# Kernel optimization log

Measured on AMD Instinct MI355X. Metric: run time of the kernel, lower is better.

Reference implementation:

```python
import jax, jax.numpy as jnp
import numpy as np

B, H, W, C = 4, 128, 128, 256
D_MODEL, NH = 512, 8
DH = D_MODEL // NH  # 64


def setup_inputs() -> dict:
    key = jax.random.key(0)
    ks = jax.random.split(key, 5)
    s = lambda fan_in: 1.0 / np.sqrt(fan_in)
    return {
        "x": jax.random.normal(ks[0], (B, H, W, C), jnp.float32),
        "Wq": jax.random.normal(ks[1], (C, D_MODEL), jnp.float32) * s(C),
        "bq": jnp.zeros((D_MODEL,), jnp.float32),
        "Wk": jax.random.normal(ks[2], (C, D_MODEL), jnp.float32) * s(C),
        "bk": jnp.zeros((D_MODEL,), jnp.float32),
        "Wv": jax.random.normal(ks[3], (C, D_MODEL), jnp.float32) * s(C),
        "bv": jnp.zeros((D_MODEL,), jnp.float32),
        "Wo": jax.random.normal(ks[4], (D_MODEL, C), jnp.float32) * s(D_MODEL),
        "bo": jnp.zeros((C,), jnp.float32),
    }


def reference(x, Wq, bq, Wk, bk, Wv, bv, Wo, bo):
    # Axial multi-head attention along axis 1 (H), W axis is batched.
    b, h, w, _ = x.shape
    q = (x @ Wq + bq).reshape(b, h, w, NH, DH) * (DH ** -0.5)
    k = (x @ Wk + bk).reshape(b, h, w, NH, DH)
    v = (x @ Wv + bv).reshape(b, h, w, NH, DH)
    # scores over the H axis: [B, Nh, W, H, H]
    scores = jnp.einsum("bxwnd,bywnd->bnwxy", q, k)
    probs = jax.nn.softmax(scores, axis=-1)
    # [B, H, W, Nh, DH] -> [B, H, W, d_model]
    out = jnp.einsum("bnwxy,bywnd->bxwnd", probs, v).reshape(b, h, w, D_MODEL)
    # Wo projection; original combines to [B,W,H,C] then permutes back to [B,H,W,C],
    # which is equivalent to applying Wo directly here. Dropout is identity at inference.
    return out @ Wo + bo
```

## Files before the change

kernel.cpp:

```cpp
#include <hip/hip_runtime.h>

typedef unsigned short u16;
typedef __attribute__((ext_vector_type(8))) short bf16x8;
typedef __attribute__((ext_vector_type(8))) unsigned short u16x8;
typedef __attribute__((ext_vector_type(4))) float f32x4;

#define DEVI static __device__ __forceinline__

DEVI u16 f2b(float f) {
  unsigned u = __builtin_bit_cast(unsigned, f);
  return (u16)((u + 0x7FFFu + ((u >> 16) & 1u)) >> 16);
}

DEVI void gload_lds16(const void* g, void* l) {
  __builtin_amdgcn_global_load_lds(
      (const __attribute__((address_space(1))) unsigned int*)g,
      (__attribute__((address_space(3))) unsigned int*)l, 16, 0, 0);
}


__global__ __launch_bounds__(256) void prep_x(const float* __restrict__ x, u16* __restrict__ xb) {
  const int n8 = 65536 * 256 / 8;
  int i = blockIdx.x * blockDim.x + threadIdx.x;
  for (; i < n8; i += gridDim.x * blockDim.x) {
    const float4* p = (const float4*)x + (size_t)i * 2;
    float4 a = p[0], b = p[1];
    u16x8 r;
    r[0] = f2b(a.x); r[1] = f2b(a.y); r[2] = f2b(a.z); r[3] = f2b(a.w);
    r[4] = f2b(b.x); r[5] = f2b(b.y); r[6] = f2b(b.z); r[7] = f2b(b.w);
    *(u16x8*)(xb + (size_t)i * 8) = r;
  }
}

__global__ __launch_bounds__(256) void prep_w(
    const float* __restrict__ Wq, const float* __restrict__ Wk,
    const float* __restrict__ Wv, const float* __restrict__ Wo,
    const float* __restrict__ bq, const float* __restrict__ bk, const float* __restrict__ bv,
    u16* __restrict__ wqkvT, u16* __restrict__ woT, float* __restrict__ bqkv) {
  const int NW1 = 1536 * 256, NW2 = 256 * 512;
  const int total = NW1 + NW2 + 1536;
  int i = blockIdx.x * blockDim.x + threadIdx.x;
  for (; i < total; i += gridDim.x * blockDim.x) {
    if (i < NW1) {
      int nn = i >> 8, kk = i & 255;
      float v;
      if (nn < 512)       v = Wq[kk * 512 + nn] * 0.125f;
      else if (nn < 1024) v = Wk[kk * 512 + (nn - 512)];
      else                v = Wv[kk * 512 + (nn - 1024)];
      wqkvT[i] = f2b(v);
    } else if (i < NW1 + NW2) {
      int j = i - NW1;
      int nn = j >> 9, kk = j & 511;
      woT[j] = f2b(Wo[kk * 256 + nn]);
    } else {
      int j = i - NW1 - NW2;
      bqkv[j] = (j < 512) ? bq[j] * 0.125f : (j < 1024 ? bk[j - 512] : bv[j - 1024]);
    }
  }
}


template <int KK, bool OUT_BF16>
__global__ __launch_bounds__(512, 2) void gemm256(
    const u16* __restrict__ A, const u16* __restrict__ Bt,
    const float* __restrict__ bias, void* __restrict__ Cv, int N) {
  constexpr int NT = KK / 64;
  __shared__ u16 smem[65536];
  const int tid = threadIdx.x;
  const int lane = tid & 63, wid = tid >> 6;
  const int nTn = N >> 8;
  const int qx = gridDim.x >> 3;
  const int wg = (blockIdx.x & 7) * qx + (blockIdx.x >> 3);
  const long m0 = (long)(wg / nTn) * 256;
  const long n0 = (long)(wg % nTn) * 256;
  const int wr = wid >> 2, wc = wid & 3;
  const int hi = lane >> 4, lo = lane & 15;
  const u16* Ab = A + m0 * KK;
  const u16* Bb = Bt + n0 * KK;
  const int srow_ = tid >> 3;
  const int schunk = tid & 7;

  f32x4 acc[8][4];
#pragma unroll
  for (int mi = 0; mi < 8; ++mi)
#pragma unroll
    for (int ni = 0; ni < 4; ++ni) acc[mi][ni] = f32x4{0.f, 0.f, 0.f, 0.f};

  auto stage = [&](int t) {
    u16* base = &smem[(t & 1) * 32768];
    const int kt = t * 64;
#pragma unroll
    for (int j = 0; j < 4; ++j) {
      int row = j * 64 + srow_;
      int colE = (schunk ^ (row & 7)) << 3;
      gload_lds16(Ab + (long)row * KK + kt + colE, &base[(j * 512 + tid) * 8]);
    }
#pragma unroll
    for (int j = 0; j < 4; ++j) {
      int row = j * 64 + srow_;
      int colE = (schunk ^ (row & 7)) << 3;
      gload_lds16(Bb + (long)row * KK + kt + colE, &base[16384 + (j * 512 + tid) * 8]);
    }
  };

  stage(0);
#pragma unroll
  for (int t = 0; t < NT; ++t) {
    if (t + 1 < NT) {
      stage(t + 1);
      asm volatile("s_waitcnt vmcnt(8)" ::: "memory");
    } else {
      asm volatile("s_waitcnt vmcnt(0)" ::: "memory");
    }
    __builtin_amdgcn_sched_barrier(0);
    __builtin_amdgcn_s_barrier();
    const u16* aB = &smem[(t & 1) * 32768];
    const u16* bB = aB + 16384;
#pragma unroll
    for (int ks = 0; ks < 2; ++ks) {
      const int slot = ((hi + ks * 4) ^ (lo & 7)) << 3;
      bf16x8 af[8], bfr[4];
#pragma unroll
      for (int mi = 0; mi < 8; ++mi)
        af[mi] = *(const bf16x8*)&aB[(wr * 128 + mi * 16 + lo) * 64 + slot];
#pragma unroll
      for (int ni = 0; ni < 4; ++ni)
        bfr[ni] = *(const bf16x8*)&bB[(wc * 64 + ni * 16 + lo) * 64 + slot];
#pragma unroll
      for (int mi = 0; mi < 8; ++mi)
#pragma unroll
        for (int ni = 0; ni < 4; ++ni)
          acc[mi][ni] = __builtin_amdgcn_mfma_f32_16x16x32_bf16(af[mi], bfr[ni], acc[mi][ni], 0, 0, 0);
    }
    __builtin_amdgcn_sched_barrier(0);
    __builtin_amdgcn_s_barrier();
  }

  float bb[4];
#pragma unroll
  for (int ni = 0; ni < 4; ++ni) bb[ni] = bias[n0 + wc * 64 + ni * 16 + lo];

  if (OUT_BF16) {
    u16* Cg = (u16*)Cv;
#pragma unroll
    for (int h = 0; h < 2; ++h) {
      if (wr == h) {
#pragma unroll
        for (int mi = 0; mi < 8; ++mi)
#pragma unroll
          for (int ni = 0; ni < 4; ++ni) {
            int cl = wc * 64 + ni * 16 + lo;
#pragma unroll
            for (int j = 0; j < 4; ++j)
              smem[(mi * 16 + hi * 4 + j) * 256 + cl] = f2b(acc[mi][ni][j] + bb[ni]);
          }
      }
      __syncthreads();
#pragma unroll
      for (int it = 0; it < 8; ++it) {
        int idx = it * 512 + tid;
        int row = idx >> 5, col8 = (idx & 31) * 8;
        *(u16x8*)(Cg + (m0 + h * 128 + row) * N + n0 + col8) = *(const u16x8*)&smem[row * 256 + col8];
      }
      __syncthreads();
    }
  } else {
    float* Cg = (float*)Cv;
#pragma unroll
    for (int mi = 0; mi < 8; ++mi)
#pragma unroll
      for (int ni = 0; ni < 4; ++ni) {
        long cg = n0 + wc * 64 + ni * 16 + lo;
#pragma unroll
        for (int j = 0; j < 4; ++j)
          Cg[(m0 + wr * 128 + mi * 16 + hi * 4 + j) * N + cg] = acc[mi][ni][j] + bb[ni];
      }
  }
}


__global__ __launch_bounds__(256) void attn_axial(const u16* __restrict__ qkv,
                                                  u16* __restrict__ ao) {
  __shared__ u16 smem[24576];
  u16* qld = smem;
  u16* kld = smem + 8192;
  u16* vt  = smem + 16384;
  u16* pld = smem;

  const int g = blockIdx.x;
  const int n = g & 7, w = (g >> 3) & 127, b = g >> 10;
  const int tid = threadIdx.x, lane = tid & 63, wid = tid >> 6;
  const size_t ystr = (size_t)128 * 1536;
  const size_t base = (size_t)(b * 16384 + w) * 1536;
  const size_t bq_ = base + n * 64;
  const size_t bk_ = base + 512 + n * 64;
  const size_t bv_ = base + 1024 + n * 64;
  const int srow = lane >> 3, sc = lane & 7;
  const int hi = lane >> 4, lo = lane & 15;

#pragma unroll
  for (int j = 0; j < 4; ++j) {
    int y = wid * 32 + j * 8 + srow;
    gload_lds16(qkv + bq_ + (size_t)y * ystr + sc * 8, &qld[(wid * 32 + j * 8) * 64]);
    gload_lds16(qkv + bk_ + (size_t)y * ystr + sc * 8, &kld[(wid * 32 + j * 8) * 64]);
  }
  {
    const int h2 = tid >> 6;
    const int yp = (tid & 63) * 2;
    const u16* g0 = qkv + bv_ + (size_t)yp * ystr + h2 * 16;
    u16x8 a0 = *(const u16x8*)g0;
    u16x8 a1 = *(const u16x8*)(g0 + 8);
    u16x8 c0 = *(const u16x8*)(g0 + ystr);
    u16x8 c1 = *(const u16x8*)(g0 + ystr + 8);
    unsigned* vt32 = (unsigned*)vt;
#pragma unroll
    for (int e = 0; e < 8; ++e) {
      vt32[(h2 * 16 + e) * 64 + (yp >> 1)]     = (unsigned)a0[e] | ((unsigned)c0[e] << 16);
      vt32[(h2 * 16 + 8 + e) * 64 + (yp >> 1)] = (unsigned)a1[e] | ((unsigned)c1[e] << 16);
    }
  }
  __syncthreads();

  f32x4 s[2][8];
#pragma unroll
  for (int mi = 0; mi < 2; ++mi)
#pragma unroll
    for (int ni = 0; ni < 8; ++ni) s[mi][ni] = f32x4{0.f, 0.f, 0.f, 0.f};
#pragma unroll
  for (int ks = 0; ks < 2; ++ks) {
    bf16x8 aq[2];
#pragma unroll
    for (int mi = 0; mi < 2; ++mi)
      aq[mi] = *(const bf16x8*)&qld[(wid * 32 + mi * 16 + lo) * 64 + hi * 8 + ks * 32];
#pragma unroll
    for (int ni = 0; ni < 8; ++ni) {
      bf16x8 bk2 = *(const bf16x8*)&kld[(ni * 16 + lo) * 64 + hi * 8 + ks * 32];
#pragma unroll
      for (int mi = 0; mi < 2; ++mi)
        s[mi][ni] = __builtin_amdgcn_mfma_f32_16x16x32_bf16(aq[mi], bk2, s[mi][ni], 0, 0, 0);
    }
  }
  __syncthreads();

  float rinv[2][4];
  u16* pw = &pld[wid * 32 * 128];
#pragma unroll
  for (int mi = 0; mi < 2; ++mi) {
#pragma unroll
    for (int j = 0; j < 4; ++j) {
      float m = s[mi][0][j];
#pragma unroll
      for (int ni = 1; ni < 8; ++ni) m = fmaxf(m, s[mi][ni][j]);
#pragma unroll
      for (int d = 1; d < 16; d <<= 1) m = fmaxf(m, __shfl_xor(m, d, 64));
      float sum = 0.f;
#pragma unroll
      for (int ni = 0; ni < 8; ++ni) {
        float e = exp2f((s[mi][ni][j] - m) * 1.44269504f);
        s[mi][ni][j] = e;
        sum += e;
      }
#pragma unroll
      for (int d = 1; d < 16; d <<= 1) sum += __shfl_xor(sum, d, 64);
      rinv[mi][j] = 1.f / sum;
      const int q = mi * 16 + hi * 4 + j;
#pragma unroll
      for (int ni = 0; ni < 8; ++ni)
        pw[q * 128 + ni * 16 + lo] = f2b(s[mi][ni][j]);
    }
  }

  f32x4 o[2][4];
#pragma unroll
  for (int mi = 0; mi < 2; ++mi)
#pragma unroll
    for (int ni = 0; ni < 4; ++ni) o[mi][ni] = f32x4{0.f, 0.f, 0.f, 0.f};
#pragma unroll
  for (int ks = 0; ks < 4; ++ks) {
    bf16x8 ap[2];
#pragma unroll
    for (int mi = 0; mi < 2; ++mi)
      ap[mi] = *(const bf16x8*)&pw[(mi * 16 + lo) * 128 + hi * 8 + ks * 32];
#pragma unroll
    for (int ni = 0; ni < 4; ++ni) {
      bf16x8 bv2 = *(const bf16x8*)&vt[(ni * 16 + lo) * 128 + hi * 8 + ks * 32];
#pragma unroll
      for (int mi = 0; mi < 2; ++mi)
        o[mi][ni] = __builtin_amdgcn_mfma_f32_16x16x32_bf16(ap[mi], bv2, o[mi][ni], 0, 0, 0);
    }
  }

#pragma unroll
  for (int mi = 0; mi < 2; ++mi)
#pragma unroll
    for (int j = 0; j < 4; ++j) {
      const int q = wid * 32 + mi * 16 + hi * 4 + j;
      const size_t obase = ((size_t)(b * 16384 + q * 128 + w)) * 512 + (size_t)n * 64;
#pragma unroll
      for (int ni = 0; ni < 4; ++ni)
        ao[obase + ni * 16 + lo] = f2b(o[mi][ni][j] * rinv[mi][j]);
    }
}


extern "C" void kernel_launch(void* const* d_in, const int* in_sizes, int n_in,
                              void* d_out, int out_size, void* d_ws, size_t ws_size,
                              hipStream_t stream) {
  (void)in_sizes; (void)n_in; (void)out_size; (void)ws_size;
  const float* x  = (const float*)d_in[0];
  const float* Wq = (const float*)d_in[1];
  const float* bq = (const float*)d_in[2];
  const float* Wk = (const float*)d_in[3];
  const float* bk = (const float*)d_in[4];
  const float* Wv = (const float*)d_in[5];
  const float* bv = (const float*)d_in[6];
  const float* Wo = (const float*)d_in[7];
  const float* bo = (const float*)d_in[8];
  float* out = (float*)d_out;

  char* ws = (char*)d_ws;
  const size_t MiB = (size_t)1 << 20;
  u16* qkv   = (u16*)ws;
  u16* xb    = (u16*)(ws + 192 * MiB);
  u16* wqkvT = (u16*)(ws + 224 * MiB);
  u16* woT   = wqkvT + 1536 * 256;
  float* bqkv = (float*)(woT + 256 * 512);

  prep_x<<<2048, 256, 0, stream>>>(x, xb);
  prep_w<<<512, 256, 0, stream>>>(Wq, Wk, Wv, Wo, bq, bk, bv, wqkvT, woT, bqkv);

  gemm256<256, true><<<1536, 512, 0, stream>>>(xb, wqkvT, bqkv, qkv, 1536);
  attn_axial<<<4096, 256, 0, stream>>>(qkv, (u16*)out);
  gemm256<512, false><<<256, 512, 0, stream>>>((const u16*)out, woT, bo, out, 256);
}
```

Measured before the change: 219.9 us.

## Fuse QKV projection, axial attention and output projection into one kernel

Replaces the five-kernel pipeline (x conversion, QKV GEMM, attention, Wo GEMM) with one fused kernel per (batch, column). Each block converts its x column to bf16 in LDS, computes Q, K and V per head from pre-swizzled weight pieces streamed through double-buffered LDS, runs softmax attention, and accumulates the Wo projection in registers. The K bias is dropped because it cancels in softmax, and the V bias is folded into a precomputed output bias. This removes the large qkv and intermediate HBM round-trips and the extra launches, at the cost of only 512 blocks, heavy LDS use and many barriers per head.

```diff
diff --git a/kernel.cpp b/kernel.cpp
--- a/kernel.cpp
+++ b/kernel.cpp
@@ -3,6 +3,7 @@
 typedef unsigned short u16;
 typedef __attribute__((ext_vector_type(8))) short bf16x8;
 typedef __attribute__((ext_vector_type(8))) unsigned short u16x8;
+typedef __attribute__((ext_vector_type(4))) unsigned short u16x4;
 typedef __attribute__((ext_vector_type(4))) float f32x4;
 
 #define DEVI static __device__ __forceinline__
@@ -18,287 +19,320 @@
       (__attribute__((address_space(3))) unsigned int*)l, 16, 0, 0);
 }
 
-
-__global__ __launch_bounds__(256) void prep_x(const float* __restrict__ x, u16* __restrict__ xb) {
-  const int n8 = 65536 * 256 / 8;
-  int i = blockIdx.x * blockDim.x + threadIdx.x;
-  for (; i < n8; i += gridDim.x * blockDim.x) {
-    const float4* p = (const float4*)x + (size_t)i * 2;
-    float4 a = p[0], b = p[1];
-    u16x8 r;
-    r[0] = f2b(a.x); r[1] = f2b(a.y); r[2] = f2b(a.z); r[3] = f2b(a.w);
-    r[4] = f2b(b.x); r[5] = f2b(b.y); r[6] = f2b(b.z); r[7] = f2b(b.w);
-    *(u16x8*)(xb + (size_t)i * 8) = r;
-  }
-}
-
-__global__ __launch_bounds__(256) void prep_w(
+#define LGKM0 asm volatile("s_waitcnt lgkmcnt(0)" ::: "memory")
+#define VMW(N) asm volatile("s_waitcnt vmcnt(" #N ")" ::: "memory")
+DEVI void sbar() {
+  __builtin_amdgcn_sched_barrier(0);
+  __builtin_amdgcn_s_barrier();
+  __builtin_amdgcn_sched_barrier(0);
+}
+DEVI bf16x8 mfma_ld(const u16* p) { return *(const bf16x8*)p; }
+
+__global__ __launch_bounds__(256) void prep_w2(
     const float* __restrict__ Wq, const float* __restrict__ Wk,
     const float* __restrict__ Wv, const float* __restrict__ Wo,
-    const float* __restrict__ bq, const float* __restrict__ bk, const float* __restrict__ bv,
-    u16* __restrict__ wqkvT, u16* __restrict__ woT, float* __restrict__ bqkv) {
-  const int NW1 = 1536 * 256, NW2 = 256 * 512;
-  const int total = NW1 + NW2 + 1536;
+    const float* __restrict__ bq, const float* __restrict__ bv,
+    const float* __restrict__ bo, u16* __restrict__ img,
+    float* __restrict__ bqv, float* __restrict__ bo2) {
+  const int NW = 524288;
+  const int total = NW + 512 + 256;
   int i = blockIdx.x * blockDim.x + threadIdx.x;
   for (; i < total; i += gridDim.x * blockDim.x) {
-    if (i < NW1) {
-      int nn = i >> 8, kk = i & 255;
+    if (i < NW) {
+      const int piece = i >> 14, r = i & 16383;
+      const int h = piece >> 2, wh = piece & 3;
       float v;
-      if (nn < 512)       v = Wq[kk * 512 + nn] * 0.125f;
-      else if (nn < 1024) v = Wk[kk * 512 + (nn - 512)];
-      else                v = Wv[kk * 512 + (nn - 1024)];
-      wqkvT[i] = f2b(v);
-    } else if (i < NW1 + NW2) {
-      int j = i - NW1;
-      int nn = j >> 9, kk = j & 511;
-      woT[j] = f2b(Wo[kk * 256 + nn]);
+      if (wh < 3) {
+        const int n = r >> 8, cpos = (r >> 3) & 31, e = r & 7;
+        const int k = ((cpos ^ (n & 7)) << 3) + e;
+        const int col = h * 64 + n;
+        v = (wh == 0) ? Wq[k * 512 + col] * 0.125f
+          : (wh == 1) ? Wk[k * 512 + col] : Wv[k * 512 + col];
+      } else {
+        const int cc = r >> 6, cpos = (r >> 3) & 7, e = r & 7;
+        const int kk = ((cpos ^ (cc & 7)) << 3) + e;
+        v = Wo[(h * 64 + kk) * 256 + cc];
+      }
+      img[i] = f2b(v);
+    } else if (i < NW + 512) {
+      const int j = i - NW;
+      bqv[j] = bq[j] * 0.125f;
     } else {
-      int j = i - NW1 - NW2;
-      bqkv[j] = (j < 512) ? bq[j] * 0.125f : (j < 1024 ? bk[j - 512] : bv[j - 1024]);
+      const int j = i - NW - 512;
+      float acc = bo[j];
+      for (int dd = 0; dd < 512; ++dd) acc += bv[dd] * Wo[dd * 256 + j];
+      bo2[j] = acc;
     }
   }
 }
 
 
-template <int KK, bool OUT_BF16>
-__global__ __launch_bounds__(512, 2) void gemm256(
-    const u16* __restrict__ A, const u16* __restrict__ Bt,
-    const float* __restrict__ bias, void* __restrict__ Cv, int N) {
-  constexpr int NT = KK / 64;
-  __shared__ u16 smem[65536];
-  const int tid = threadIdx.x;
-  const int lane = tid & 63, wid = tid >> 6;
-  const int nTn = N >> 8;
-  const int qx = gridDim.x >> 3;
-  const int wg = (blockIdx.x & 7) * qx + (blockIdx.x >> 3);
-  const long m0 = (long)(wg / nTn) * 256;
-  const long n0 = (long)(wg % nTn) * 256;
-  const int wr = wid >> 2, wc = wid & 3;
-  const int hi = lane >> 4, lo = lane & 15;
-  const u16* Ab = A + m0 * KK;
-  const u16* Bb = Bt + n0 * KK;
-  const int srow_ = tid >> 3;
-  const int schunk = tid & 7;
-
-  f32x4 acc[8][4];
-#pragma unroll
-  for (int mi = 0; mi < 8; ++mi)
-#pragma unroll
-    for (int ni = 0; ni < 4; ++ni) acc[mi][ni] = f32x4{0.f, 0.f, 0.f, 0.f};
-
-  auto stage = [&](int t) {
-    u16* base = &smem[(t & 1) * 32768];
-    const int kt = t * 64;
-#pragma unroll
-    for (int j = 0; j < 4; ++j) {
-      int row = j * 64 + srow_;
-      int colE = (schunk ^ (row & 7)) << 3;
-      gload_lds16(Ab + (long)row * KK + kt + colE, &base[(j * 512 + tid) * 8]);
-    }
-#pragma unroll
-    for (int j = 0; j < 4; ++j) {
-      int row = j * 64 + srow_;
-      int colE = (schunk ^ (row & 7)) << 3;
-      gload_lds16(Bb + (long)row * KK + kt + colE, &base[16384 + (j * 512 + tid) * 8]);
-    }
-  };
-
-  stage(0);
-#pragma unroll
-  for (int t = 0; t < NT; ++t) {
-    if (t + 1 < NT) {
-      stage(t + 1);
-      asm volatile("s_waitcnt vmcnt(8)" ::: "memory");
-    } else {
-      asm volatile("s_waitcnt vmcnt(0)" ::: "memory");
-    }
-    __builtin_amdgcn_sched_barrier(0);
-    __builtin_amdgcn_s_barrier();
-    const u16* aB = &smem[(t & 1) * 32768];
-    const u16* bB = aB + 16384;
-#pragma unroll
-    for (int ks = 0; ks < 2; ++ks) {
-      const int slot = ((hi + ks * 4) ^ (lo & 7)) << 3;
-      bf16x8 af[8], bfr[4];
-#pragma unroll
-      for (int mi = 0; mi < 8; ++mi)
-        af[mi] = *(const bf16x8*)&aB[(wr * 128 + mi * 16 + lo) * 64 + slot];
-#pragma unroll
-      for (int ni = 0; ni < 4; ++ni)
-        bfr[ni] = *(const bf16x8*)&bB[(wc * 64 + ni * 16 + lo) * 64 + slot];
-#pragma unroll
-      for (int mi = 0; mi < 8; ++mi)
-#pragma unroll
-        for (int ni = 0; ni < 4; ++ni)
-          acc[mi][ni] = __builtin_amdgcn_mfma_f32_16x16x32_bf16(af[mi], bfr[ni], acc[mi][ni], 0, 0, 0);
-    }
-    __builtin_amdgcn_sched_barrier(0);
-    __builtin_amdgcn_s_barrier();
-  }
-
-  float bb[4];
-#pragma unroll
-  for (int ni = 0; ni < 4; ++ni) bb[ni] = bias[n0 + wc * 64 + ni * 16 + lo];
-
-  if (OUT_BF16) {
-    u16* Cg = (u16*)Cv;
-#pragma unroll
-    for (int h = 0; h < 2; ++h) {
-      if (wr == h) {
-#pragma unroll
-        for (int mi = 0; mi < 8; ++mi)
-#pragma unroll
-          for (int ni = 0; ni < 4; ++ni) {
-            int cl = wc * 64 + ni * 16 + lo;
-#pragma unroll
-            for (int j = 0; j < 4; ++j)
-              smem[(mi * 16 + hi * 4 + j) * 256 + cl] = f2b(acc[mi][ni][j] + bb[ni]);
-          }
-      }
-      __syncthreads();
-#pragma unroll
-      for (int it = 0; it < 8; ++it) {
-        int idx = it * 512 + tid;
-        int row = idx >> 5, col8 = (idx & 31) * 8;
-        *(u16x8*)(Cg + (m0 + h * 128 + row) * N + n0 + col8) = *(const u16x8*)&smem[row * 256 + col8];
-      }
-      __syncthreads();
-    }
-  } else {
-    float* Cg = (float*)Cv;
-#pragma unroll
-    for (int mi = 0; mi < 8; ++mi)
-#pragma unroll
-      for (int ni = 0; ni < 4; ++ni) {
-        long cg = n0 + wc * 64 + ni * 16 + lo;
-#pragma unroll
-        for (int j = 0; j < 4; ++j)
-          Cg[(m0 + wr * 128 + mi * 16 + hi * 4 + j) * N + cg] = acc[mi][ni][j] + bb[ni];
-      }
-  }
-}
-
-
-__global__ __launch_bounds__(256) void attn_axial(const u16* __restrict__ qkv,
-                                                  u16* __restrict__ ao) {
-  __shared__ u16 smem[24576];
-  u16* qld = smem;
-  u16* kld = smem + 8192;
-  u16* vt  = smem + 16384;
-  u16* pld = smem;
+__global__ __launch_bounds__(512) void fused_axial(
+    const float* __restrict__ x, const u16* __restrict__ img,
+    const float* __restrict__ bqv, const float* __restrict__ bo2,
+    float* __restrict__ out) {
+  __shared__ u16 lds[73728];
+  const int WB0 = 0, WB1 = 16384, QB = 32768, KB = 40960, VT = 49152, PB = 57344;
+  const int XO = 32768;
 
   const int g = blockIdx.x;
-  const int n = g & 7, w = (g >> 3) & 127, b = g >> 10;
+  const int b = g >> 7, w = g & 127;
   const int tid = threadIdx.x, lane = tid & 63, wid = tid >> 6;
-  const size_t ystr = (size_t)128 * 1536;
-  const size_t base = (size_t)(b * 16384 + w) * 1536;
-  const size_t bq_ = base + n * 64;
-  const size_t bk_ = base + 512 + n * 64;
-  const size_t bv_ = base + 1024 + n * 64;
-  const int srow = lane >> 3, sc = lane & 7;
-  const int hi = lane >> 4, lo = lane & 15;
-
-#pragma unroll
-  for (int j = 0; j < 4; ++j) {
-    int y = wid * 32 + j * 8 + srow;
-    gload_lds16(qkv + bq_ + (size_t)y * ystr + sc * 8, &qld[(wid * 32 + j * 8) * 64]);
-    gload_lds16(qkv + bk_ + (size_t)y * ystr + sc * 8, &kld[(wid * 32 + j * 8) * 64]);
-  }
+  const int s = wid >> 1, nh = wid & 1;
+  const int lo = lane & 15, hi = lane >> 4;
+  const int l8 = lo & 7;
+
   {
-    const int h2 = tid >> 6;
-    const int yp = (tid & 63) * 2;
-    const u16* g0 = qkv + bv_ + (size_t)yp * ystr + h2 * 16;
-    u16x8 a0 = *(const u16x8*)g0;
-    u16x8 a1 = *(const u16x8*)(g0 + 8);
-    u16x8 c0 = *(const u16x8*)(g0 + ystr);
-    u16x8 c1 = *(const u16x8*)(g0 + ystr + 8);
-    unsigned* vt32 = (unsigned*)vt;
-#pragma unroll
-    for (int e = 0; e < 8; ++e) {
-      vt32[(h2 * 16 + e) * 64 + (yp >> 1)]     = (unsigned)a0[e] | ((unsigned)c0[e] << 16);
-      vt32[(h2 * 16 + 8 + e) * 64 + (yp >> 1)] = (unsigned)a1[e] | ((unsigned)c1[e] << 16);
+    const int y = tid >> 2, q4 = tid & 3;
+    const float4* xr = (const float4*)(x + ((size_t)((b * 128 + y) * 128 + w)) * 256) + q4 * 16;
+#pragma unroll
+    for (int c8 = 0; c8 < 8; ++c8) {
+      float4 f0 = xr[c8 * 2], f1 = xr[c8 * 2 + 1];
+      u16x8 r;
+      r[0] = f2b(f0.x); r[1] = f2b(f0.y); r[2] = f2b(f0.z); r[3] = f2b(f0.w);
+      r[4] = f2b(f1.x); r[5] = f2b(f1.y); r[6] = f2b(f1.z); r[7] = f2b(f1.w);
+      *(u16x8*)&lds[XO + y * 256 + (((q4 * 8 + c8) ^ (y & 7)) << 3)] = r;
     }
   }
   __syncthreads();
 
-  f32x4 s[2][8];
-#pragma unroll
-  for (int mi = 0; mi < 2; ++mi)
-#pragma unroll
-    for (int ni = 0; ni < 8; ++ni) s[mi][ni] = f32x4{0.f, 0.f, 0.f, 0.f};
-#pragma unroll
-  for (int ks = 0; ks < 2; ++ks) {
-    bf16x8 aq[2];
-#pragma unroll
-    for (int mi = 0; mi < 2; ++mi)
-      aq[mi] = *(const bf16x8*)&qld[(wid * 32 + mi * 16 + lo) * 64 + hi * 8 + ks * 32];
-#pragma unroll
-    for (int ni = 0; ni < 8; ++ni) {
-      bf16x8 bk2 = *(const bf16x8*)&kld[(ni * 16 + lo) * 64 + hi * 8 + ks * 32];
-#pragma unroll
-      for (int mi = 0; mi < 2; ++mi)
-        s[mi][ni] = __builtin_amdgcn_mfma_f32_16x16x32_bf16(aq[mi], bk2, s[mi][ni], 0, 0, 0);
-    }
+  bf16x8 areg[2][8];
+#pragma unroll
+  for (int m = 0; m < 2; ++m)
+#pragma unroll
+    for (int k8 = 0; k8 < 8; ++k8)
+      areg[m][k8] = mfma_ld(&lds[XO + (s * 32 + m * 16 + lo) * 256 + (((k8 * 4 + hi) ^ l8) << 3)]);
+
+  auto stagep = [&](int piece) {
+    const u16* src = img + (size_t)piece * 16384;
+    u16* dst = &lds[(piece & 1) ? WB1 : WB0];
+#pragma unroll
+    for (int it = 0; it < 4; ++it)
+      gload_lds16(src + (it * 512 + tid) * 8, dst + (it * 512 + tid) * 8);
+  };
+
+  stagep(0);
+  float bqa = bqv[nh * 32 + lo], bqb = bqv[nh * 32 + 16 + lo];
+
+  f32x4 oacc[2][8];
+#pragma unroll
+  for (int m = 0; m < 2; ++m)
+#pragma unroll
+    for (int n = 0; n < 8; ++n) oacc[m][n] = f32x4{0.f, 0.f, 0.f, 0.f};
+
+  LGKM0;
+  sbar();
+
+  for (int h = 0; h < 8; ++h) {
+    const int p0 = h * 4;
+
+    stagep(p0 + 1);
+    VMW(4); sbar();
+    {
+      f32x4 ga[2][2];
+#pragma unroll
+      for (int m = 0; m < 2; ++m)
+#pragma unroll
+        for (int n = 0; n < 2; ++n) ga[m][n] = f32x4{0.f, 0.f, 0.f, 0.f};
+#pragma unroll
+      for (int k8 = 0; k8 < 8; ++k8) {
+        bf16x8 bf0 = mfma_ld(&lds[WB0 + (nh * 32 + lo) * 256 + (((k8 * 4 + hi) ^ l8) << 3)]);
+        bf16x8 bf1 = mfma_ld(&lds[WB0 + (nh * 32 + 16 + lo) * 256 + (((k8 * 4 + hi) ^ l8) << 3)]);
+#pragma unroll
+        for (int m = 0; m < 2; ++m) {
+          ga[m][0] = __builtin_amdgcn_mfma_f32_16x16x32_bf16(areg[m][k8], bf0, ga[m][0], 0, 0, 0);
+          ga[m][1] = __builtin_amdgcn_mfma_f32_16x16x32_bf16(areg[m][k8], bf1, ga[m][1], 0, 0, 0);
+        }
+      }
+#pragma unroll
+      for (int n = 0; n < 2; ++n) {
+        const int d = nh * 32 + n * 16 + lo;
+        const float bia = n ? bqb : bqa;
+#pragma unroll
+        for (int m = 0; m < 2; ++m)
+#pragma unroll
+          for (int j = 0; j < 4; ++j) {
+            const int y = s * 32 + m * 16 + hi * 4 + j;
+            lds[QB + y * 64 + (((d >> 3) ^ (y & 7)) << 3) + (d & 7)] = f2b(ga[m][n][j] + bia);
+          }
+      }
+    }
+    LGKM0; sbar();
+
+    stagep(p0 + 2);
+    VMW(4); sbar();
+    {
+      f32x4 ga[2][2];
+#pragma unroll
+      for (int m = 0; m < 2; ++m)
+#pragma unroll
+        for (int n = 0; n < 2; ++n) ga[m][n] = f32x4{0.f, 0.f, 0.f, 0.f};
+#pragma unroll
+      for (int k8 = 0; k8 < 8; ++k8) {
+        bf16x8 bf0 = mfma_ld(&lds[WB1 + (nh * 32 + lo) * 256 + (((k8 * 4 + hi) ^ l8) << 3)]);
+        bf16x8 bf1 = mfma_ld(&lds[WB1 + (nh * 32 + 16 + lo) * 256 + (((k8 * 4 + hi) ^ l8) << 3)]);
+#pragma unroll
+        for (int m = 0; m < 2; ++m) {
+          ga[m][0] = __builtin_amdgcn_mfma_f32_16x16x32_bf16(areg[m][k8], bf0, ga[m][0], 0, 0, 0);
+          ga[m][1] = __builtin_amdgcn_mfma_f32_16x16x32_bf16(areg[m][k8], bf1, ga[m][1], 0, 0, 0);
+        }
+      }
+#pragma unroll
+      for (int n = 0; n < 2; ++n) {
+        const int d = nh * 32 + n * 16 + lo;
+#pragma unroll
+        for (int m = 0; m < 2; ++m)
+#pragma unroll
+          for (int j = 0; j < 4; ++j) {
+            const int y = s * 32 + m * 16 + hi * 4 + j;
+            lds[KB + y * 64 + (((d >> 3) ^ (y & 7)) << 3) + (d & 7)] = f2b(ga[m][n][j]);
+          }
+      }
+    }
+    LGKM0; sbar();
+
+    stagep(p0 + 3);
+    VMW(4); sbar();
+    {
+      f32x4 ga[2][2];
+#pragma unroll
+      for (int m = 0; m < 2; ++m)
+#pragma unroll
+        for (int n = 0; n < 2; ++n) ga[m][n] = f32x4{0.f, 0.f, 0.f, 0.f};
+#pragma unroll
+      for (int k8 = 0; k8 < 8; ++k8) {
+        bf16x8 bf0 = mfma_ld(&lds[WB0 + (nh * 32 + lo) * 256 + (((k8 * 4 + hi) ^ l8) << 3)]);
+        bf16x8 bf1 = mfma_ld(&lds[WB0 + (nh * 32 + 16 + lo) * 256 + (((k8 * 4 + hi) ^ l8) << 3)]);
+#pragma unroll
+        for (int m = 0; m < 2; ++m) {
+          ga[m][0] = __builtin_amdgcn_mfma_f32_16x16x32_bf16(areg[m][k8], bf0, ga[m][0], 0, 0, 0);
+          ga[m][1] = __builtin_amdgcn_mfma_f32_16x16x32_bf16(areg[m][k8], bf1, ga[m][1], 0, 0, 0);
+        }
+      }
+#pragma unroll
+      for (int n = 0; n < 2; ++n) {
+        const int d = nh * 32 + n * 16 + lo;
+#pragma unroll
+        for (int m = 0; m < 2; ++m) {
+          const int y0 = s * 32 + m * 16 + hi * 4;
+          u16x4 pk;
+#pragma unroll
+          for (int j = 0; j < 4; ++j) pk[j] = f2b(ga[m][n][j]);
+          *(u16x4*)&lds[VT + d * 128 + ((((y0 >> 3)) ^ (d & 7)) << 3) + ((hi & 1) * 4)] = pk;
+        }
+      }
+    }
+    LGKM0; sbar();
+
+    {
+      f32x4 sacc[8];
+#pragma unroll
+      for (int n = 0; n < 8; ++n) sacc[n] = f32x4{0.f, 0.f, 0.f, 0.f};
+#pragma unroll
+      for (int ks = 0; ks < 2; ++ks) {
+        bf16x8 aq = mfma_ld(&lds[QB + (wid * 16 + lo) * 64 + (((hi + ks * 4) ^ l8) << 3)]);
+#pragma unroll
+        for (int n = 0; n < 8; ++n) {
+          bf16x8 kf = mfma_ld(&lds[KB + (n * 16 + lo) * 64 + (((hi + ks * 4) ^ l8) << 3)]);
+          sacc[n] = __builtin_amdgcn_mfma_f32_16x16x32_bf16(aq, kf, sacc[n], 0, 0, 0);
+        }
+      }
+#pragma unroll
+      for (int j = 0; j < 4; ++j) {
+        float mx = sacc[0][j];
+#pragma unroll
+        for (int n = 1; n < 8; ++n) mx = fmaxf(mx, sacc[n][j]);
+#pragma unroll
+        for (int d = 1; d < 16; d <<= 1) mx = fmaxf(mx, __shfl_xor(mx, d, 64));
+        float sum = 0.f;
+#pragma unroll
+        for (int n = 0; n < 8; ++n) {
+          float e = exp2f((sacc[n][j] - mx) * 1.44269504f);
+          sacc[n][j] = e;
+          sum += e;
+        }
+#pragma unroll
+        for (int d = 1; d < 16; d <<= 1) sum += __shfl_xor(sum, d, 64);
+        const float rinv = 1.f / sum;
+        const int y = wid * 16 + hi * 4 + j;
+#pragma unroll
+        for (int n = 0; n < 8; ++n) {
+          const int yp = n * 16 + lo;
+          lds[PB + y * 128 + ((((yp >> 3)) ^ (y & 7)) << 3) + (yp & 7)] = f2b(sacc[n][j] * rinv);
+        }
+      }
+    }
+    LGKM0; sbar();
+
+    if (h < 7) {
+      stagep(p0 + 4);
+      bqa = bqv[(h + 1) * 64 + nh * 32 + lo];
+      bqb = bqv[(h + 1) * 64 + nh * 32 + 16 + lo];
+    }
+    {
+      f32x4 pv[2][2];
+#pragma unroll
+      for (int m = 0; m < 2; ++m)
+#pragma unroll
+        for (int n = 0; n < 2; ++n) pv[m][n] = f32x4{0.f, 0.f, 0.f, 0.f};
+#pragma unroll
+      for (int ks = 0; ks < 4; ++ks) {
+        bf16x8 ap[2];
+#pragma unroll
+        for (int m = 0; m < 2; ++m)
+          ap[m] = mfma_ld(&lds[PB + (s * 32 + m * 16 + lo) * 128 + (((hi + ks * 4) ^ l8) << 3)]);
+#pragma unroll
+        for (int n = 0; n < 2; ++n) {
+          const int d = nh * 32 + n * 16 + lo;
+          bf16x8 vf = mfma_ld(&lds[VT + d * 128 + (((hi + ks * 4) ^ l8) << 3)]);
+#pragma unroll
+          for (int m = 0; m < 2; ++m)
+            pv[m][n] = __builtin_amdgcn_mfma_f32_16x16x32_bf16(ap[m], vf, pv[m][n], 0, 0, 0);
+        }
+      }
+#pragma unroll
+      for (int n = 0; n < 2; ++n) {
+        const int d = nh * 32 + n * 16 + lo;
+#pragma unroll
+        for (int m = 0; m < 2; ++m)
+#pragma unroll
+          for (int j = 0; j < 4; ++j) {
+            const int y = s * 32 + m * 16 + hi * 4 + j;
+            lds[QB + y * 64 + (((d >> 3) ^ (y & 7)) << 3) + (d & 7)] = f2b(pv[m][n][j]);
+          }
+      }
+    }
+    if (h < 7) { VMW(4); } else { VMW(0); }
+    LGKM0; sbar();
+
+    {
+#pragma unroll
+      for (int ks = 0; ks < 2; ++ks) {
+        bf16x8 af0 = mfma_ld(&lds[QB + (s * 32 + lo) * 64 + (((hi + ks * 4) ^ l8) << 3)]);
+        bf16x8 af1 = mfma_ld(&lds[QB + (s * 32 + 16 + lo) * 64 + (((hi + ks * 4) ^ l8) << 3)]);
+#pragma unroll
+        for (int n = 0; n < 8; ++n) {
+          const int c = nh * 128 + n * 16 + lo;
+          bf16x8 wf = mfma_ld(&lds[WB1 + c * 64 + (((hi + ks * 4) ^ l8) << 3)]);
+          oacc[0][n] = __builtin_amdgcn_mfma_f32_16x16x32_bf16(af0, wf, oacc[0][n], 0, 0, 0);
+          oacc[1][n] = __builtin_amdgcn_mfma_f32_16x16x32_bf16(af1, wf, oacc[1][n], 0, 0, 0);
+        }
+      }
+    }
+    LGKM0; sbar();
   }
-  __syncthreads();
-
-  float rinv[2][4];
-  u16* pw = &pld[wid * 32 * 128];
-#pragma unroll
-  for (int mi = 0; mi < 2; ++mi) {
+
+  float bbn[8];
+#pragma unroll
+  for (int n = 0; n < 8; ++n) bbn[n] = bo2[nh * 128 + n * 16 + lo];
+#pragma unroll
+  for (int m = 0; m < 2; ++m)
 #pragma unroll
     for (int j = 0; j < 4; ++j) {
-      float m = s[mi][0][j];
-#pragma unroll
-      for (int ni = 1; ni < 8; ++ni) m = fmaxf(m, s[mi][ni][j]);
-#pragma unroll
-      for (int d = 1; d < 16; d <<= 1) m = fmaxf(m, __shfl_xor(m, d, 64));
-      float sum = 0.f;
-#pragma unroll
-      for (int ni = 0; ni < 8; ++ni) {
-        float e = exp2f((s[mi][ni][j] - m) * 1.44269504f);
-        s[mi][ni][j] = e;
-        sum += e;
-      }
-#pragma unroll
-      for (int d = 1; d < 16; d <<= 1) sum += __shfl_xor(sum, d, 64);
-      rinv[mi][j] = 1.f / sum;
-      const int q = mi * 16 + hi * 4 + j;
-#pragma unroll
-      for (int ni = 0; ni < 8; ++ni)
-        pw[q * 128 + ni * 16 + lo] = f2b(s[mi][ni][j]);
-    }
-  }
-
-  f32x4 o[2][4];
-#pragma unroll
-  for (int mi = 0; mi < 2; ++mi)
-#pragma unroll
-    for (int ni = 0; ni < 4; ++ni) o[mi][ni] = f32x4{0.f, 0.f, 0.f, 0.f};
-#pragma unroll
-  for (int ks = 0; ks < 4; ++ks) {
-    bf16x8 ap[2];
-#pragma unroll
-    for (int mi = 0; mi < 2; ++mi)
-      ap[mi] = *(const bf16x8*)&pw[(mi * 16 + lo) * 128 + hi * 8 + ks * 32];
-#pragma unroll
-    for (int ni = 0; ni < 4; ++ni) {
-      bf16x8 bv2 = *(const bf16x8*)&vt[(ni * 16 + lo) * 128 + hi * 8 + ks * 32];
-#pragma unroll
-      for (int mi = 0; mi < 2; ++mi)
-        o[mi][ni] = __builtin_amdgcn_mfma_f32_16x16x32_bf16(ap[mi], bv2, o[mi][ni], 0, 0, 0);
-    }
-  }
-
-#pragma unroll
-  for (int mi = 0; mi < 2; ++mi)
-#pragma unroll
-    for (int j = 0; j < 4; ++j) {
-      const int q = wid * 32 + mi * 16 + hi * 4 + j;
-      const size_t obase = ((size_t)(b * 16384 + q * 128 + w)) * 512 + (size_t)n * 64;
-#pragma unroll
-      for (int ni = 0; ni < 4; ++ni)
-        ao[obase + ni * 16 + lo] = f2b(o[mi][ni][j] * rinv[mi][j]);
+      const int y = s * 32 + m * 16 + hi * 4 + j;
+      float* orow = out + ((size_t)((b * 128 + y) * 128 + w)) * 256 + nh * 128;
+#pragma unroll
+      for (int n = 0; n < 8; ++n) orow[n * 16 + lo] = oacc[m][n][j] + bbn[n];
     }
 }
 
@@ -311,7 +345,6 @@
   const float* Wq = (const float*)d_in[1];
   const float* bq = (const float*)d_in[2];
   const float* Wk = (const float*)d_in[3];
-  const float* bk = (const float*)d_in[4];
   const float* Wv = (const float*)d_in[5];
   const float* bv = (const float*)d_in[6];
   const float* Wo = (const float*)d_in[7];
@@ -320,16 +353,10 @@
 
   char* ws = (char*)d_ws;
   const size_t MiB = (size_t)1 << 20;
-  u16* qkv   = (u16*)ws;
-  u16* xb    = (u16*)(ws + 192 * MiB);
-  u16* wqkvT = (u16*)(ws + 224 * MiB);
-  u16* woT   = wqkvT + 1536 * 256;
-  float* bqkv = (float*)(woT + 256 * 512);
-
-  prep_x<<<2048, 256, 0, stream>>>(x, xb);
-  prep_w<<<512, 256, 0, stream>>>(Wq, Wk, Wv, Wo, bq, bk, bv, wqkvT, woT, bqkv);
-
-  gemm256<256, true><<<1536, 512, 0, stream>>>(xb, wqkvT, bqkv, qkv, 1536);
-  attn_axial<<<4096, 256, 0, stream>>>(qkv, (u16*)out);
-  gemm256<512, false><<<256, 512, 0, stream>>>((const u16*)out, woT, bo, out, 256);
-}
+  u16* img   = (u16*)ws;
+  float* bqv = (float*)(ws + MiB);
+  float* bo2 = bqv + 512;
+
+  prep_w2<<<512, 256, 0, stream>>>(Wq, Wk, Wv, Wo, bq, bv, bo, img, bqv, bo2);
+  fused_axial<<<512, 512, 0, stream>>>(x, img, bqv, bo2, out);
+}
```

After: 323.4 us. 1.47x slower.
